# Performance work log

Measured on AMD Instinct MI355X. Metric: run time of the kernel, lower is better.

## Reference

```python
import jax, jax.numpy as jnp
import numpy as np

B = 2_000_000
ND = 3

def _skew(v):
    # v: [B,3] -> [B,3,3] skew-symmetric matrix
    z = jnp.zeros_like(v[..., 0])
    r0 = jnp.stack([z, -v[..., 2], v[..., 1]], axis=-1)
    r1 = jnp.stack([v[..., 2], z, -v[..., 0]], axis=-1)
    r2 = jnp.stack([-v[..., 1], v[..., 0], z], axis=-1)
    return jnp.stack([r0, r1, r2], axis=-2)

def _rotmat(v):
    # Closed-form expm of skew(v) (Rodrigues). Mathematically identical to tf.linalg.expm.
    th2 = jnp.sum(v * v, axis=-1)                      # [B]
    th = jnp.sqrt(th2)
    small = th < 1e-6
    th_s = jnp.where(small, 1.0, th)
    th2_s = jnp.where(small, 1.0, th2)
    a = jnp.where(small, 1.0, jnp.sin(th) / th_s)      # sin(t)/t
    b = jnp.where(small, 0.5, (1.0 - jnp.cos(th)) / th2_s)  # (1-cos t)/t^2
    K = _skew(v)                                       # [B,3,3]
    I = jnp.eye(ND, dtype=v.dtype)
    return I + a[:, None, None] * K + b[:, None, None] * jnp.matmul(K, K)

def setup_inputs() -> dict:
    key = jax.random.key(0)
    k1, k2, k3, k4 = jax.random.split(key, 4)
    trans = jax.random.normal(k1, (B, ND), dtype=jnp.float32)
    rotat = jax.random.normal(k2, (B, ND), dtype=jnp.float32)
    scal_dir = jax.random.normal(k3, (B, ND), dtype=jnp.float32)
    scal = jax.random.normal(k4, (B, ND), dtype=jnp.float32)
    return {"trans": trans, "rotat": rotat, "scal_dir": scal_dir, "scal": scal}

def reference(trans, rotat, scal_dir, scal):
    R = _rotmat(rotat)          # [B,3,3] rotation
    U = _rotmat(scal_dir)       # [B,3,3] scaling direction
    D = jnp.exp(scal)           # expm(diag(s)) == diag(exp(s)), [B,3]
    # U @ diag(D) @ U^T, then R @ (.)
    Ut = jnp.swapaxes(U, -1, -2)
    M = jnp.matmul(U, D[:, :, None] * Ut)   # diag(D) @ U^T broadcast as row-scaling
    M = jnp.matmul(R, M)
    return jnp.concatenate([M, trans[:, :, None]], axis=2)  # [B,3,4]
```

## Files before the change

### kernel.cpp

```cpp
#include <hip/hip_runtime.h>
#include <math.h>

#define TPB 256

__device__ __forceinline__ void rodrigues(float v0, float v1, float v2, float R[9]) {
    float th2 = v0 * v0 + v1 * v1 + v2 * v2;
    bool  sm  = th2 < 1e-12f;
    float g   = sm ? 1.0f : th2;
    float inv = rsqrtf(g);
    float th  = g * inv;
    float s   = __sinf(th);
    float c   = __cosf(th);
    float a   = sm ? 1.0f : s * inv;
    float b   = sm ? 0.5f : (1.0f - c) * (inv * inv);
    float cc  = 1.0f - b * th2;
    R[0] = cc + b * v0 * v0;      R[1] = b * v0 * v1 - a * v2;  R[2] = b * v0 * v2 + a * v1;
    R[3] = b * v0 * v1 + a * v2;  R[4] = cc + b * v1 * v1;      R[5] = b * v1 * v2 - a * v0;
    R[6] = b * v0 * v2 - a * v1;  R[7] = b * v1 * v2 + a * v0;  R[8] = cc + b * v2 * v2;
}

__global__ __launch_bounds__(TPB) void aff_kernel(
    const float* __restrict__ trans,
    const float* __restrict__ rotat,
    const float* __restrict__ sdir,
    const float* __restrict__ scal,
    float4* __restrict__ out,
    int B)
{
    __shared__ float4 s_out[TPB / 64][192];

    const int tid   = threadIdx.x;
    const int w     = tid >> 6;
    const int l     = tid & 63;
    const int ebase = blockIdx.x * TPB + (w << 6);
    if (ebase >= B) return;
    const int e  = ebase + l;
    const int b3 = 3 * e;

    float t0 = trans[b3], t1 = trans[b3 + 1], t2 = trans[b3 + 2];
    float r0 = rotat[b3], r1 = rotat[b3 + 1], r2 = rotat[b3 + 2];
    float u0 = sdir [b3], u1 = sdir [b3 + 1], u2 = sdir [b3 + 2];
    float s0 = scal [b3], s1 = scal [b3 + 1], s2 = scal [b3 + 2];

    float R[9], U[9];
    rodrigues(r0, r1, r2, R);
    rodrigues(u0, u1, u2, U);
    float d0 = __expf(s0);
    float d1 = __expf(s1);
    float d2 = __expf(s2);

    float W[9];
#pragma unroll
    for (int i = 0; i < 3; ++i) {
        W[3*i+0] = U[3*i+0] * d0;
        W[3*i+1] = U[3*i+1] * d1;
        W[3*i+2] = U[3*i+2] * d2;
    }
    float S[9];
#pragma unroll
    for (int i = 0; i < 3; ++i)
#pragma unroll
        for (int j = 0; j < 3; ++j)
            S[3*i+j] = W[3*i+0]*U[3*j+0] + W[3*i+1]*U[3*j+1] + W[3*i+2]*U[3*j+2];
    float M[9];
#pragma unroll
    for (int i = 0; i < 3; ++i)
#pragma unroll
        for (int j = 0; j < 3; ++j)
            M[3*i+j] = R[3*i+0]*S[0+j] + R[3*i+1]*S[3+j] + R[3*i+2]*S[6+j];

    float4* slab = s_out[w];
    slab[3*l + 0] = make_float4(M[0], M[1], M[2], t0);
    slab[3*l + 1] = make_float4(M[3], M[4], M[5], t1);
    slab[3*l + 2] = make_float4(M[6], M[7], M[8], t2);

    __builtin_amdgcn_wave_barrier();

    const int ob = 3 * ebase;
#pragma unroll
    for (int k = 0; k < 3; ++k) {
        int idx = (k << 6) + l;
        out[ob + idx] = slab[idx];
    }
}

extern "C" void kernel_launch(void* const* d_in, const int* in_sizes, int n_in,
                              void* d_out, int out_size, void* d_ws, size_t ws_size,
                              hipStream_t stream) {
    const float* tr = (const float*)d_in[0];
    const float* ro = (const float*)d_in[1];
    const float* sd = (const float*)d_in[2];
    const float* sc = (const float*)d_in[3];
    float4* out = (float4*)d_out;

    int B = in_sizes[0] / 3;
    int blocks = (B + TPB - 1) / TPB;
    aff_kernel<<<blocks, TPB, 0, stream>>>(tr, ro, sd, sc, out, B);
}
```

Baseline: 176.8 us.

## Make kernel persistent with grid-stride loop and register prefetch of next tile

```diff
diff --git a/kernel.cpp b/kernel.cpp
--- a/kernel.cpp
+++ b/kernel.cpp
@@ -2,6 +2,8 @@
 #include <math.h>
 
 #define TPB 256
+#define WPW (TPB / 64)
+#define NBLOCKS 1024
 
 __device__ __forceinline__ void rodrigues(float v0, float v1, float v2, float R[9]) {
     float th2 = v0 * v0 + v1 * v1 + v2 * v2;
@@ -19,68 +21,87 @@
     R[6] = b * v0 * v2 - a * v1;  R[7] = b * v1 * v2 + a * v0;  R[8] = cc + b * v2 * v2;
 }
 
+__device__ __forceinline__ void load12(const float* __restrict__ trans,
+                                       const float* __restrict__ rotat,
+                                       const float* __restrict__ sdir,
+                                       const float* __restrict__ scal,
+                                       int b3, float p[12]) {
+    p[0] = trans[b3]; p[1]  = trans[b3+1]; p[2]  = trans[b3+2];
+    p[3] = rotat[b3]; p[4]  = rotat[b3+1]; p[5]  = rotat[b3+2];
+    p[6] = sdir [b3]; p[7]  = sdir [b3+1]; p[8]  = sdir [b3+2];
+    p[9] = scal [b3]; p[10] = scal [b3+1]; p[11] = scal [b3+2];
+}
+
 __global__ __launch_bounds__(TPB) void aff_kernel(
     const float* __restrict__ trans,
     const float* __restrict__ rotat,
     const float* __restrict__ sdir,
     const float* __restrict__ scal,
     float4* __restrict__ out,
-    int B)
+    int T)
 {
-    __shared__ float4 s_out[TPB / 64][192];
+    __shared__ float4 s_out[WPW][192];
+    const int w   = threadIdx.x >> 6;
+    const int l   = threadIdx.x & 63;
+    float4* slab  = s_out[w];
+    const int wid = blockIdx.x * WPW + w;
+    const int W   = gridDim.x * WPW;
 
-    const int tid   = threadIdx.x;
-    const int w     = tid >> 6;
-    const int l     = tid & 63;
-    const int ebase = blockIdx.x * TPB + (w << 6);
-    if (ebase >= B) return;
-    const int e  = ebase + l;
-    const int b3 = 3 * e;
+    int t = wid;
+    if (t >= T) return;
 
-    float t0 = trans[b3], t1 = trans[b3 + 1], t2 = trans[b3 + 2];
-    float r0 = rotat[b3], r1 = rotat[b3 + 1], r2 = rotat[b3 + 2];
-    float u0 = sdir [b3], u1 = sdir [b3 + 1], u2 = sdir [b3 + 2];
-    float s0 = scal [b3], s1 = scal [b3 + 1], s2 = scal [b3 + 2];
+    float p[12];
+    load12(trans, rotat, sdir, scal, 3 * ((t << 6) + l), p);
 
-    float R[9], U[9];
-    rodrigues(r0, r1, r2, R);
-    rodrigues(u0, u1, u2, U);
-    float d0 = __expf(s0);
-    float d1 = __expf(s1);
-    float d2 = __expf(s2);
+    while (true) {
+        float c[12];
+#pragma unroll
+        for (int i = 0; i < 12; ++i) c[i] = p[i];
 
-    float W[9];
+        const int tn = t + W;
+        if (tn < T) load12(trans, rotat, sdir, scal, 3 * ((tn << 6) + l), p);
+
+        float R[9], U[9];
+        rodrigues(c[3], c[4], c[5], R);
+        rodrigues(c[6], c[7], c[8], U);
+        float d0 = __expf(c[9]);
+        float d1 = __expf(c[10]);
+        float d2 = __expf(c[11]);
+
+        float Wm[9];
 #pragma unroll
-    for (int i = 0; i < 3; ++i) {
-        W[3*i+0] = U[3*i+0] * d0;
-        W[3*i+1] = U[3*i+1] * d1;
-        W[3*i+2] = U[3*i+2] * d2;
-    }
-    float S[9];
+        for (int i = 0; i < 3; ++i) {
+            Wm[3*i+0] = U[3*i+0] * d0;
+            Wm[3*i+1] = U[3*i+1] * d1;
+            Wm[3*i+2] = U[3*i+2] * d2;
+        }
+        float S[9];
 #pragma unroll
-    for (int i = 0; i < 3; ++i)
+        for (int i = 0; i < 3; ++i)
 #pragma unroll
-        for (int j = 0; j < 3; ++j)
-            S[3*i+j] = W[3*i+0]*U[3*j+0] + W[3*i+1]*U[3*j+1] + W[3*i+2]*U[3*j+2];
-    float M[9];
+            for (int j = 0; j < 3; ++j)
+                S[3*i+j] = Wm[3*i+0]*U[3*j+0] + Wm[3*i+1]*U[3*j+1] + Wm[3*i+2]*U[3*j+2];
+        float M[9];
 #pragma unroll
-    for (int i = 0; i < 3; ++i)
+        for (int i = 0; i < 3; ++i)
 #pragma unroll
-        for (int j = 0; j < 3; ++j)
-            M[3*i+j] = R[3*i+0]*S[0+j] + R[3*i+1]*S[3+j] + R[3*i+2]*S[6+j];
+            for (int j = 0; j < 3; ++j)
+                M[3*i+j] = R[3*i+0]*S[0+j] + R[3*i+1]*S[3+j] + R[3*i+2]*S[6+j];
 
-    float4* slab = s_out[w];
-    slab[3*l + 0] = make_float4(M[0], M[1], M[2], t0);
-    slab[3*l + 1] = make_float4(M[3], M[4], M[5], t1);
-    slab[3*l + 2] = make_float4(M[6], M[7], M[8], t2);
+        slab[3*l + 0] = make_float4(M[0], M[1], M[2], c[0]);
+        slab[3*l + 1] = make_float4(M[3], M[4], M[5], c[1]);
+        slab[3*l + 2] = make_float4(M[6], M[7], M[8], c[2]);
+        __builtin_amdgcn_wave_barrier();
 
-    __builtin_amdgcn_wave_barrier();
+        const int ob = 192 * t;
+#pragma unroll
+        for (int k = 0; k < 3; ++k) {
+            int idx = (k << 6) + l;
+            out[ob + idx] = slab[idx];
+        }
 
-    const int ob = 3 * ebase;
-#pragma unroll
-    for (int k = 0; k < 3; ++k) {
-        int idx = (k << 6) + l;
-        out[ob + idx] = slab[idx];
+        if (tn >= T) break;
+        t = tn;
     }
 }
 
@@ -94,6 +115,8 @@
     float4* out = (float4*)d_out;
 
     int B = in_sizes[0] / 3;
-    int blocks = (B + TPB - 1) / TPB;
-    aff_kernel<<<blocks, TPB, 0, stream>>>(tr, ro, sd, sc, out, B);
+    int T = B >> 6;
+    int blocks = NBLOCKS;
+    if (blocks * WPW > T) blocks = (T + WPW - 1) / WPW;
+    aff_kernel<<<blocks, TPB, 0, stream>>>(tr, ro, sd, sc, out, T);
 }
```

Result: no change. 177.5 us (+0.4%).
